# Optimization experiments

Measured on AMD Instinct MI355X. Metric: run time of the kernel, lower is better.

The kernel has to match this reference:

```python
import jax, jax.numpy as jnp
import numpy as np

B, C, D = 256, 50000, 512
ALPHA = 0.5


def setup_inputs() -> dict:
    key = jax.random.key(0)
    k1, k2, k3 = jax.random.split(key, 3)
    x = jax.random.normal(k1, (B, D), dtype=jnp.float32)
    labels = jax.random.randint(k2, (B,), 0, C)
    onehot = jax.nn.one_hot(labels, C, dtype=jnp.float32)  # [B, C]
    # 'uniform' keras initializer -> U(-0.05, 0.05)
    centers = jax.random.uniform(k3, (C, D), dtype=jnp.float32, minval=-0.05, maxval=0.05)
    return {"x": x, "onehot": onehot, "centers": centers}


def reference(x, onehot, centers):
    # gather-as-matmul: selected center per sample, [B, D]
    sel = jnp.matmul(onehot, centers)
    # scatter-add-as-matmul: per-class accumulated delta, [C, D]
    delta_centers = jnp.matmul(onehot.T, sel - x)
    # per-class counts (+1), [C, 1]
    center_counts = jnp.sum(onehot.T, axis=1, keepdims=True) + 1.0
    delta_centers = delta_centers / center_counts
    new_centers = centers - ALPHA * delta_centers
    # squared distance to (old) center, [B, 1]
    diff = x - sel
    result = jnp.sum(diff * diff, axis=1, keepdims=True)
    return result, new_centers
```

## Files before the change

### kernel.cpp

```cpp
#include <hip/hip_runtime.h>

#define B_N 256
#define C_N 50000
#define D_N 512
#define ALPHA 0.5f

__global__ __launch_bounds__(256) void find_labels(
        const float* __restrict__ onehot,
        int* __restrict__ labels,
        int* __restrict__ counts) {
    int t = threadIdx.x;
    int base = blockIdx.x * 1024 + t;
    const float4* p = (const float4*)onehot;
    float4 v[4];
#pragma unroll
    for (int k = 0; k < 4; ++k) v[k] = p[base + k * 256];
#pragma unroll
    for (int k = 0; k < 4; ++k) {
        float4 q = v[k];
        if (q.x != 0.f || q.y != 0.f || q.z != 0.f || q.w != 0.f) {
            int g = (base + k * 256) * 4;
            float f[4] = {q.x, q.y, q.z, q.w};
#pragma unroll
            for (int j = 0; j < 4; ++j) {
                if (f[j] != 0.f) {
                    int gg = g + j;
                    int b = gg / C_N;
                    int c = gg - b * C_N;
                    labels[b] = c;
                    atomicAdd(&counts[c], 1);
                }
            }
        }
    }
}

__global__ __launch_bounds__(128) void sq_dist(
        const float* __restrict__ x,
        const float* __restrict__ centers,
        const int* __restrict__ labels,
        float* __restrict__ result) {
    int b = blockIdx.x;
    int t = threadIdx.x;
    int lab = labels[b];
    float4 xv = ((const float4*)(x + (size_t)b * D_N))[t];
    float4 cv = ((const float4*)(centers + (size_t)lab * D_N))[t];
    float dx = xv.x - cv.x, dy = xv.y - cv.y, dz = xv.z - cv.z, dw = xv.w - cv.w;
    float s = dx * dx + dy * dy + dz * dz + dw * dw;
#pragma unroll
    for (int off = 32; off > 0; off >>= 1) s += __shfl_down(s, off, 64);
    __shared__ float ws[2];
    if ((t & 63) == 0) ws[t >> 6] = s;
    __syncthreads();
    if (t == 0) result[b] = ws[0] + ws[1];
}

__global__ __launch_bounds__(256) void update_centers(
        const float* __restrict__ x,
        const float* __restrict__ centers,
        const int* __restrict__ labels,
        const int* __restrict__ counts,
        float* __restrict__ newc) {
    int t = threadIdx.x;
    int half = t >> 7;
    int tt = t & 127;
    const float4* c4 = (const float4*)centers;
    float4* n4 = (float4*)newc;
    for (int base = blockIdx.x * 8; base < C_N; base += gridDim.x * 8) {
        int row[4], cnt[4];
        float4 cv[4];
#pragma unroll
        for (int k = 0; k < 4; ++k) row[k] = base + 2 * k + half;
#pragma unroll
        for (int k = 0; k < 4; ++k) cnt[k] = counts[row[k]];
#pragma unroll
        for (int k = 0; k < 4; ++k) cv[k] = c4[(size_t)row[k] * 128 + tt];
#pragma unroll
        for (int k = 0; k < 4; ++k) {
            int n = cnt[k];
            float4 res;
            if (n == 0) {
                res = cv[k];
            } else {
                int c = row[k];
                float4 sx = make_float4(0.f, 0.f, 0.f, 0.f);
                for (int b = 0; b < B_N; ++b) {
                    if (labels[b] == c) {
                        float4 xv = ((const float4*)(x + (size_t)b * D_N))[tt];
                        sx.x += xv.x; sx.y += xv.y; sx.z += xv.z; sx.w += xv.w;
                    }
                }
                float inv = 1.0f / (float)(n + 1);
                float ac = 1.0f - ALPHA * (float)n * inv;
                float bc = ALPHA * inv;
                res.x = cv[k].x * ac + sx.x * bc;
                res.y = cv[k].y * ac + sx.y * bc;
                res.z = cv[k].z * ac + sx.z * bc;
                res.w = cv[k].w * ac + sx.w * bc;
            }
            n4[(size_t)row[k] * 128 + tt] = res;
        }
    }
}

extern "C" void kernel_launch(void* const* d_in, const int* in_sizes, int n_in,
                              void* d_out, int out_size, void* d_ws, size_t ws_size,
                              hipStream_t stream) {
    const float* x       = (const float*)d_in[0];
    const float* onehot  = (const float*)d_in[1];
    const float* centers = (const float*)d_in[2];
    float* out    = (float*)d_out;
    float* result = out;
    float* newc   = out + B_N;

    int* counts = (int*)d_ws;
    int* labels = counts + C_N;

    hipMemsetAsync(counts, 0, C_N * sizeof(int), stream);

    find_labels<<<(B_N * C_N / 4) / 1024, 256, 0, stream>>>(onehot, labels, counts);
    sq_dist<<<B_N, 128, 0, stream>>>(x, centers, labels, result);
    update_centers<<<2048, 256, 0, stream>>>(x, centers, labels, counts, newc);
}
```

Baseline: 243.9 us.

## Replace per-row center update with bulk copy plus per-label fixup kernel

The per-class counts array, its memset and the atomics are removed. New centers are first filled by a plain vectorized copy of the old centers, and then only the rows whose class appears in the batch are recomputed by a small per-sample kernel. That kernel dedupes classes by letting only the first sample carrying a label write the row. The bulk copy is meant to cut the per-row count branching and scheduling overhead of the old grid-stride update, at the cost of one extra kernel launch and a write-after-write ordering dependency between the copy and the fixup.

New measurement: 244.7 us. Within noise of the previous version (+0.3%).

```diff
diff --git a/kernel.cpp b/kernel.cpp
--- a/kernel.cpp
+++ b/kernel.cpp
@@ -5,10 +5,22 @@
 #define D_N 512
 #define ALPHA 0.5f
 
+__global__ __launch_bounds__(256) void copy_centers(
+        const float4* __restrict__ src, float4* __restrict__ dst) {
+    int base = blockIdx.x * 1024 + threadIdx.x;
+    float4 v0 = src[base];
+    float4 v1 = src[base + 256];
+    float4 v2 = src[base + 512];
+    float4 v3 = src[base + 768];
+    dst[base]       = v0;
+    dst[base + 256] = v1;
+    dst[base + 512] = v2;
+    dst[base + 768] = v3;
+}
+
 __global__ __launch_bounds__(256) void find_labels(
         const float* __restrict__ onehot,
-        int* __restrict__ labels,
-        int* __restrict__ counts) {
+        int* __restrict__ labels) {
     int t = threadIdx.x;
     int base = blockIdx.x * 1024 + t;
     const float4* p = (const float4*)onehot;
@@ -28,7 +40,6 @@
                     int b = gg / C_N;
                     int c = gg - b * C_N;
                     labels[b] = c;
-                    atomicAdd(&counts[c], 1);
                 }
             }
         }
@@ -55,52 +66,44 @@
     if (t == 0) result[b] = ws[0] + ws[1];
 }
 
-__global__ __launch_bounds__(256) void update_centers(
+__global__ __launch_bounds__(128) void fixup_touched(
         const float* __restrict__ x,
         const float* __restrict__ centers,
         const int* __restrict__ labels,
-        const int* __restrict__ counts,
         float* __restrict__ newc) {
+    __shared__ int sl[B_N];
     int t = threadIdx.x;
-    int half = t >> 7;
-    int tt = t & 127;
-    const float4* c4 = (const float4*)centers;
-    float4* n4 = (float4*)newc;
-    for (int base = blockIdx.x * 8; base < C_N; base += gridDim.x * 8) {
-        int row[4], cnt[4];
-        float4 cv[4];
-#pragma unroll
-        for (int k = 0; k < 4; ++k) row[k] = base + 2 * k + half;
-#pragma unroll
-        for (int k = 0; k < 4; ++k) cnt[k] = counts[row[k]];
-#pragma unroll
-        for (int k = 0; k < 4; ++k) cv[k] = c4[(size_t)row[k] * 128 + tt];
-#pragma unroll
-        for (int k = 0; k < 4; ++k) {
-            int n = cnt[k];
-            float4 res;
-            if (n == 0) {
-                res = cv[k];
-            } else {
-                int c = row[k];
-                float4 sx = make_float4(0.f, 0.f, 0.f, 0.f);
-                for (int b = 0; b < B_N; ++b) {
-                    if (labels[b] == c) {
-                        float4 xv = ((const float4*)(x + (size_t)b * D_N))[tt];
-                        sx.x += xv.x; sx.y += xv.y; sx.z += xv.z; sx.w += xv.w;
-                    }
-                }
-                float inv = 1.0f / (float)(n + 1);
-                float ac = 1.0f - ALPHA * (float)n * inv;
-                float bc = ALPHA * inv;
-                res.x = cv[k].x * ac + sx.x * bc;
-                res.y = cv[k].y * ac + sx.y * bc;
-                res.z = cv[k].z * ac + sx.z * bc;
-                res.w = cv[k].w * ac + sx.w * bc;
-            }
-            n4[(size_t)row[k] * 128 + tt] = res;
+    int b = blockIdx.x;
+    sl[t] = labels[t];
+    sl[t + 128] = labels[t + 128];
+    __syncthreads();
+    int c = sl[b];
+    int n = 0;
+    bool canonical = true;
+    for (int i = 0; i < B_N; ++i) {
+        if (sl[i] == c) {
+            n++;
+            if (i < b) canonical = false;
         }
     }
+    if (!canonical) return;
+    float4 cv = ((const float4*)(centers + (size_t)c * D_N))[t];
+    float4 sx = make_float4(0.f, 0.f, 0.f, 0.f);
+    for (int i = 0; i < B_N; ++i) {
+        if (sl[i] == c) {
+            float4 xv = ((const float4*)(x + (size_t)i * D_N))[t];
+            sx.x += xv.x; sx.y += xv.y; sx.z += xv.z; sx.w += xv.w;
+        }
+    }
+    float inv = 1.0f / (float)(n + 1);
+    float ac = 1.0f - ALPHA * (float)n * inv;
+    float bc = ALPHA * inv;
+    float4 res;
+    res.x = cv.x * ac + sx.x * bc;
+    res.y = cv.y * ac + sx.y * bc;
+    res.z = cv.z * ac + sx.z * bc;
+    res.w = cv.w * ac + sx.w * bc;
+    ((float4*)(newc + (size_t)c * D_N))[t] = res;
 }
 
 extern "C" void kernel_launch(void* const* d_in, const int* in_sizes, int n_in,
@@ -113,12 +116,11 @@
     float* result = out;
     float* newc   = out + B_N;
 
-    int* counts = (int*)d_ws;
-    int* labels = counts + C_N;
+    int* labels = (int*)d_ws;
 
-    hipMemsetAsync(counts, 0, C_N * sizeof(int), stream);
-
-    find_labels<<<(B_N * C_N / 4) / 1024, 256, 0, stream>>>(onehot, labels, counts);
+    copy_centers<<<C_N * D_N / 4 / 1024, 256, 0, stream>>>(
+        (const float4*)centers, (float4*)newc);
+    find_labels<<<B_N * C_N / 4 / 1024, 256, 0, stream>>>(onehot, labels);
     sq_dist<<<B_N, 128, 0, stream>>>(x, centers, labels, result);
-    update_centers<<<2048, 256, 0, stream>>>(x, centers, labels, counts, newc);
+    fixup_touched<<<B_N, 128, 0, stream>>>(x, centers, labels, newc);
 }
```
